# Performance work log

Hardware: AMD Instinct MI355X
Metric: run time of the kernel (lower is better)

Reference implementation:

```python
import jax, jax.numpy as jnp
import numpy as np

NEG_SLOPE = 0.01  # torch F.leaky_relu default


def setup_inputs() -> dict:
    key = jax.random.key(0)
    k1, k2, k3, k4, k5 = jax.random.split(key, 5)
    N, E, IN_DIM, OUT_DIM = 100000, 1600000, 128, 64
    h = jax.random.normal(k1, (N, IN_DIM), dtype=jnp.float32)
    src = jax.random.randint(k2, (E,), 0, N, dtype=jnp.int64)
    dst = jax.random.randint(k3, (E,), 0, N, dtype=jnp.int64)
    # xavier_normal-ish scaled params
    W1 = jax.random.normal(k4, (OUT_DIM, IN_DIM), dtype=jnp.float32) * (2.0 / (IN_DIM + OUT_DIM)) ** 0.5
    Wa = jax.random.normal(k5, (1, 2 * OUT_DIM), dtype=jnp.float32) * (2.0 / (2 * OUT_DIM + 1)) ** 0.5
    return {"h": h, "src": src, "dst": dst, "W1": W1, "Wa": Wa}


def reference(h, src, dst, W1, Wa):
    N = h.shape[0]
    D = W1.shape[0]
    z = h @ W1.T  # [N, D]
    z_src = z[src]  # [E, D] gather
    z_dst = z[dst]  # [E, D] gather
    a_src, a_dst = Wa[0, :D], Wa[0, D:]
    # attn_fc(concat(z_src, z_dst)) == z_src@a_src + z_dst@a_dst
    e = z_src @ a_src + z_dst @ a_dst  # [E]
    e = jnp.where(e >= 0, e, NEG_SLOPE * e)  # leaky_relu
    # segment softmax over incoming edges of each dst node
    e_max = jax.ops.segment_max(e, dst, num_segments=N)
    e_max = jnp.where(jnp.isfinite(e_max), e_max, 0.0)  # empty segments
    e_exp = jnp.exp(e - e_max[dst])
    denom = jax.ops.segment_sum(e_exp, dst, num_segments=N)
    alpha = e_exp / jnp.maximum(denom, 1e-16)[dst]  # [E]
    # weighted scatter-sum of source messages
    h_out = jax.ops.segment_sum(alpha[:, None] * z_src, dst, num_segments=N)  # [N, D]
    return h_out
```

## Files before the change

kernel.cpp:

```cpp
#include <hip/hip_runtime.h>
#include <hip/hip_bf16.h>

#define NEG_SLOPE 0.01f
#define NPB 512
#define CHUNK 2048
#define GROWS 128

typedef __attribute__((ext_vector_type(8))) short short8;
typedef __attribute__((ext_vector_type(4))) float f32x4;

__device__ __forceinline__ unsigned short f2bf_rne(float f) {
    unsigned u = __float_as_uint(f);
    u += 0x7FFFu + ((u >> 16) & 1u);
    return (unsigned short)(u >> 16);
}

__global__ __launch_bounds__(256, 4) void k_gp(
    const float* __restrict__ h, const float* __restrict__ W1,
    const float* __restrict__ Wa, unsigned short* __restrict__ zb,
    float* __restrict__ s, float* __restrict__ t, int N, int G1,
    const int* __restrict__ src, const int* __restrict__ dst,
    unsigned* __restrict__ gcur, unsigned* __restrict__ table,
    int E, int NBKT, int BCAP)
{
    __shared__ __align__(16) union SM {
        struct { short wsb[64 * 128]; short tbuf[4][16 * 64]; } g;
        struct {
            unsigned cnt[256]; unsigned exc[256]; unsigned sbuf[256];
            unsigned gbaseb[256]; unsigned stage[CHUNK];
            unsigned short bkt[CHUNK];
        } p;
    } sm;
    const int tid = threadIdx.x;

    if (blockIdx.x < (unsigned)G1) {
        const int nb = blockIdx.x * GROWS;
        const int w  = tid >> 6;
        const int l  = tid & 63;
        const int lr = l & 15;
        const int lc = l >> 4;
        const int rowbase = nb + w * 32;
        const float4* __restrict__ h4 = (const float4*)h;
        const float4* __restrict__ W14 = (const float4*)W1;

        float asrc[4], adst[4];
#pragma unroll
        for (int ni = 0; ni < 4; ++ni) {
            asrc[ni] = Wa[ni * 16 + lr];
            adst[ni] = Wa[64 + ni * 16 + lr];
        }

        float4 av[8];
        {
            const int myn = rowbase + lr;
#pragma unroll
            for (int ks = 0; ks < 4; ++ks) {
                const int kcb = ks * 4 + lc;
                if (myn < N) {
                    av[2 * ks]     = h4[(size_t)myn * 32 + kcb * 2];
                    av[2 * ks + 1] = h4[(size_t)myn * 32 + kcb * 2 + 1];
                } else {
                    av[2 * ks]     = make_float4(0.f, 0.f, 0.f, 0.f);
                    av[2 * ks + 1] = make_float4(0.f, 0.f, 0.f, 0.f);
                }
            }
        }

#pragma unroll
        for (int it = 0; it < 4; ++it) {
            const int q = tid + it * 256;
            const int r = q >> 4, cb = q & 15;
            float4 v0 = W14[(size_t)r * 32 + cb * 2];
            float4 v1 = W14[(size_t)r * 32 + cb * 2 + 1];
            short8 o;
            o[0]=f2bf_rne(v0.x); o[1]=f2bf_rne(v0.y); o[2]=f2bf_rne(v0.z); o[3]=f2bf_rne(v0.w);
            o[4]=f2bf_rne(v1.x); o[5]=f2bf_rne(v1.y); o[6]=f2bf_rne(v1.z); o[7]=f2bf_rne(v1.w);
            *(short8*)&sm.g.wsb[r * 128 + ((cb * 8) ^ ((r & 7) << 3))] = o;
        }
        __syncthreads();

        short* __restrict__ tb = sm.g.tbuf[w];

#pragma unroll
        for (int rg = 0; rg < 2; ++rg) {
            short8 afr[4];
#pragma unroll
            for (int ks = 0; ks < 4; ++ks) {
                const float4 v0 = av[2 * ks], v1 = av[2 * ks + 1];
                short8 o;
                o[0]=f2bf_rne(v0.x); o[1]=f2bf_rne(v0.y); o[2]=f2bf_rne(v0.z); o[3]=f2bf_rne(v0.w);
                o[4]=f2bf_rne(v1.x); o[5]=f2bf_rne(v1.y); o[6]=f2bf_rne(v1.z); o[7]=f2bf_rne(v1.w);
                afr[ks] = o;
            }
            if (rg < 1) {
                const int myn = rowbase + 16 + lr;
#pragma unroll
                for (int ks = 0; ks < 4; ++ks) {
                    const int kcb = ks * 4 + lc;
                    if (myn < N) {
                        av[2 * ks]     = h4[(size_t)myn * 32 + kcb * 2];
                        av[2 * ks + 1] = h4[(size_t)myn * 32 + kcb * 2 + 1];
                    } else {
                        av[2 * ks]     = make_float4(0.f, 0.f, 0.f, 0.f);
                        av[2 * ks + 1] = make_float4(0.f, 0.f, 0.f, 0.f);
                    }
                }
            }

            f32x4 acc[4];
#pragma unroll
            for (int ni = 0; ni < 4; ++ni) acc[ni] = (f32x4){0.f, 0.f, 0.f, 0.f};
#pragma unroll
            for (int ks = 0; ks < 4; ++ks) {
                const int kcb = ks * 4 + lc;
#pragma unroll
                for (int ni = 0; ni < 4; ++ni) {
                    const int wr = ni * 16 + lr;
                    const short8 bf = *(const short8*)&sm.g.wsb[wr * 128 + ((kcb * 8) ^ ((wr & 7) << 3))];
                    acc[ni] = __builtin_amdgcn_mfma_f32_16x16x32_bf16(afr[ks], bf, acc[ni], 0, 0, 0);
                }
            }

#pragma unroll
            for (int r = 0; r < 4; ++r) {
                float ps = 0.f, pt = 0.f;
#pragma unroll
                for (int ni = 0; ni < 4; ++ni) {
                    ps = fmaf(acc[ni][r], asrc[ni], ps);
                    pt = fmaf(acc[ni][r], adst[ni], pt);
                }
#pragma unroll
                for (int m = 1; m < 16; m <<= 1) {
                    ps += __shfl_xor(ps, m);
                    pt += __shfl_xor(pt, m);
                }
                const int node = rowbase + rg * 16 + lc * 4 + r;
                if (lr == 0 && node < N) { s[node] = ps; t[node] = pt; }
            }

#pragma unroll
            for (int ni = 0; ni < 4; ++ni) {
                const int col = ni * 16 + lr;
#pragma unroll
                for (int r = 0; r < 4; ++r) {
                    const int ro = lc * 4 + r;
                    tb[ro * 64 + (((col >> 3) ^ (ro & 7)) << 3) + (col & 7)]
                        = (short)f2bf_rne(acc[ni][r]);
                }
            }
            {
                const int ro = l >> 2;
                const int n = rowbase + rg * 16 + ro;
                if (n < N) {
#pragma unroll
                    for (int j = 0; j < 2; ++j) {
                        const int c = (l & 3) * 2 + j;
                        const short8 v = *(const short8*)&tb[ro * 64 + ((c ^ (ro & 7)) << 3)];
                        *(short8*)&zb[(size_t)n * 64 + c * 8] = v;
                    }
                }
            }
        }
    } else {
        const int e0 = (blockIdx.x - G1) * CHUNK;
        const int nE = min(CHUNK, E - e0);

        sm.p.cnt[tid] = 0u;
        __syncthreads();
        for (int i = tid; i < nE; i += 256)
            atomicAdd(&sm.p.cnt[(unsigned)dst[e0 + i] >> 9], 1u);
        __syncthreads();

        const unsigned myc = sm.p.cnt[tid];
        if (tid < NBKT && myc > 0u) sm.p.gbaseb[tid] = atomicAdd(&gcur[tid], myc);

        sm.p.sbuf[tid] = myc;
        __syncthreads();
        for (int off = 1; off < 256; off <<= 1) {
            unsigned x = (tid >= off) ? sm.p.sbuf[tid - off] : 0u;
            __syncthreads();
            sm.p.sbuf[tid] += x;
            __syncthreads();
        }
        sm.p.exc[tid] = sm.p.sbuf[tid] - myc;
        __syncthreads();
        sm.p.cnt[tid] = 0u;
        __syncthreads();

        for (int i = tid; i < nE; i += 256) {
            const unsigned d = (unsigned)dst[e0 + i];
            const unsigned b = d >> 9;
            const unsigned pos = sm.p.exc[b] + atomicAdd(&sm.p.cnt[b], 1u);
            sm.p.stage[pos] = ((unsigned)src[e0 + i] << 9) | (d & 511u);
            sm.p.bkt[pos] = (unsigned short)b;
        }
        __syncthreads();

        for (int i = tid; i < nE; i += 256) {
            const unsigned b = sm.p.bkt[i];
            const unsigned off = sm.p.gbaseb[b] + ((unsigned)i - sm.p.exc[b]);
            if (off < (unsigned)BCAP)
                table[(size_t)b * BCAP + off] = sm.p.stage[i];
        }
    }
}

__global__ __launch_bounds__(512) void k_sp(
    const unsigned* __restrict__ table, const unsigned* __restrict__ gcur,
    const float* __restrict__ s, const float* __restrict__ t,
    uint2* __restrict__ edge_ps, unsigned* __restrict__ offsets,
    unsigned* __restrict__ counts, float* __restrict__ invden,
    int N, int NBKT, int BCAP)
{
    __shared__ unsigned ncnt[NPB], nexc[NPB], scur[NPB], sbuf[NPB];
    __shared__ float tlds[NPB], den[NPB];
    __shared__ unsigned basesh;
    const int tid = threadIdx.x;
    const int b = blockIdx.x;
    const int bc = min((int)gcur[b], BCAP);
    const size_t tbo = (size_t)b * BCAP;
    const int node = b * NPB + tid;

    {
        unsigned c = (tid < NBKT) ? min(gcur[tid], (unsigned)BCAP) : 0u;
        sbuf[tid] = c;
        __syncthreads();
        for (int off = 1; off < NPB; off <<= 1) {
            unsigned x = (tid >= off) ? sbuf[tid - off] : 0u;
            __syncthreads();
            sbuf[tid] += x;
            __syncthreads();
        }
        if (tid == 0) basesh = (b == 0) ? 0u : sbuf[b - 1];
    }
    tlds[tid] = (node < N) ? t[node] : 0.f;
    den[tid] = 0.f;
    ncnt[tid] = 0u;
    __syncthreads();
    const unsigned base = basesh;

    for (int i = tid; i < bc; i += NPB)
        atomicAdd(&ncnt[table[tbo + i] & 511u], 1u);
    __syncthreads();

    const unsigned c0 = ncnt[tid];
    sbuf[tid] = c0;
    __syncthreads();
    for (int off = 1; off < NPB; off <<= 1) {
        unsigned x = (tid >= off) ? sbuf[tid - off] : 0u;
        __syncthreads();
        sbuf[tid] += x;
        __syncthreads();
    }
    nexc[tid] = sbuf[tid] - c0;
    scur[tid] = 0u;
    __syncthreads();

    if (node < N) { offsets[node] = base + nexc[tid]; counts[node] = c0; }

    for (int i = tid; i < bc; i += NPB) {
        const unsigned v = table[tbo + i];
        const unsigned l = v & 511u;
        const unsigned sj = v >> 9;
        float e = s[sj] + tlds[l];
        e = (e >= 0.f) ? e : NEG_SLOPE * e;
        const float p = __expf(e);
        const unsigned pos = nexc[l] + atomicAdd(&scur[l], 1u);
        edge_ps[base + pos] = make_uint2(__float_as_uint(p), sj);
        atomicAdd(&den[l], p);
    }
    __syncthreads();
    if (node < N) invden[node] = 1.f / fmaxf(den[tid], 1e-16f);
}

__global__ __launch_bounds__(256) void k_node(
    const unsigned* __restrict__ offsets, const unsigned* __restrict__ counts,
    const uint2* __restrict__ edge_ps, const float* __restrict__ invden,
    const unsigned short* __restrict__ zb, float* __restrict__ out, int N)
{
    const int tid = threadIdx.x;
    const int node = blockIdx.x * 16 + (tid >> 4);
    if (node >= N) return;
    const int wl    = tid & 63;
    const int gbase = wl & ~15;
    const int sub   = wl & 15;
    const int g2    = sub >> 3;
    const int l8    = sub & 7;

    const unsigned beg = offsets[node];
    const int cnt = (int)counts[node];
    if (cnt == 0) {
        if (sub < 8) {
            const float4 zz = make_float4(0.f, 0.f, 0.f, 0.f);
            *(float4*)&out[(size_t)node * 64 + sub * 8]     = zz;
            *(float4*)&out[(size_t)node * 64 + sub * 8 + 4] = zz;
        }
        return;
    }

    const float invd = invden[node];
    const unsigned short* __restrict__ zrow = zb + l8 * 8;
    float acc[8] = {0.f, 0.f, 0.f, 0.f, 0.f, 0.f, 0.f, 0.f};

    for (int base = 0; base < cnt; base += 16) {
        const int rem = cnt - base;
        uint2 ep = make_uint2(0u, 0u);
        if (sub < rem) ep = edge_ps[beg + base + sub];
        const float p = __uint_as_float(ep.x);
        const int  sj = (int)ep.y;

        uint4 vv[8];
#pragma unroll
        for (int k = 0; k < 8; ++k) {
            const int sjj = __shfl(sj, gbase + g2 * 8 + k);
            vv[k] = *(const uint4*)&zrow[(size_t)sjj * 64];
        }
#pragma unroll
        for (int k = 0; k < 8; ++k) {
            const float pj = __shfl(p, gbase + g2 * 8 + k);
            const uint4 v = vv[k];
#define UNPK(u, d0) \
            acc[d0]     = fmaf(pj, __uint_as_float((u) << 16),          acc[d0]); \
            acc[d0 + 1] = fmaf(pj, __uint_as_float((u) & 0xFFFF0000u), acc[d0 + 1]);
            UNPK(v.x, 0) UNPK(v.y, 2) UNPK(v.z, 4) UNPK(v.w, 6)
#undef UNPK
        }
    }

#pragma unroll
    for (int c = 0; c < 8; ++c)
        acc[c] += __shfl_xor(acc[c], 8);

    if (sub < 8) {
        float4 o0 = make_float4(acc[0] * invd, acc[1] * invd, acc[2] * invd, acc[3] * invd);
        float4 o1 = make_float4(acc[4] * invd, acc[5] * invd, acc[6] * invd, acc[7] * invd);
        *(float4*)&out[(size_t)node * 64 + sub * 8]     = o0;
        *(float4*)&out[(size_t)node * 64 + sub * 8 + 4] = o1;
    }
}

extern "C" void kernel_launch(void* const* d_in, const int* in_sizes, int n_in,
                              void* d_out, int out_size, void* d_ws, size_t ws_size,
                              hipStream_t stream) {
    const float* h   = (const float*)d_in[0];
    const int*   src = (const int*)d_in[1];
    const int*   dst = (const int*)d_in[2];
    const float* W1  = (const float*)d_in[3];
    const float* Wa  = (const float*)d_in[4];
    float* out = (float*)d_out;

    const int N = in_sizes[0] / 128;
    const int E = in_sizes[1];
    const int NBKT = (N + NPB - 1) / NPB;
    const int meanb = (E + NBKT - 1) / NBKT;
    int slack = 24 * (int)sqrtf((float)meanb) + 64;
    const int BCAP = meanb + slack;

    const int G1 = (N + GROWS - 1) / GROWS;
    const int G2 = (E + CHUNK - 1) / CHUNK;

    unsigned short* zb = (unsigned short*)d_ws;
    float*    s        = (float*)(zb + (size_t)N * 64);
    float*    t        = s + N;
    unsigned* gcur     = (unsigned*)(t + N);
    unsigned* offsets  = gcur + NBKT;
    unsigned* counts   = offsets + N;
    float*    invden   = (float*)(counts + N);
    uint2*    edge_ps  = (uint2*)(invden + N);
    unsigned* table    = (unsigned*)(edge_ps + E);

    hipMemsetAsync(gcur, 0, (size_t)NBKT * sizeof(unsigned), stream);

    k_gp<<<G1 + G2, 256, 0, stream>>>(h, W1, Wa, zb, s, t, N, G1,
                                      src, dst, gcur, table, E, NBKT, BCAP);
    k_sp<<<NBKT, 512, 0, stream>>>(table, gcur, s, t, edge_ps, offsets, counts,
                                   invden, N, NBKT, BCAP);
    k_node<<<(N + 15) / 16, 256, 0, stream>>>(offsets, counts, edge_ps, invden, zb, out, N);
}
```

Measured before the change: 97.62 us.

## Interleave GEMM and partition blocks and replace LDS scans with wave shuffles

Block indices of the fused kernel now alternate between the GEMM/projection role and the edge-bucketing role, so both kinds of work run concurrently instead of in two sequential phases of the grid. The barrier-heavy Hillis-Steele shared-memory scans in both kernels become wave-level shuffle scans plus a small per-wave total combine, which cuts many __syncthreads. The launch-bounds occupancy hint on k_gp is also lowered from 4 to 2 blocks per SM, which may change register allocation.

```diff
diff --git a/kernel.cpp b/kernel.cpp
--- a/kernel.cpp
+++ b/kernel.cpp
@@ -15,26 +15,41 @@
     return (unsigned short)(u >> 16);
 }
 
-__global__ __launch_bounds__(256, 4) void k_gp(
+__device__ __forceinline__ unsigned wscan_incl(unsigned v) {
+    const int ln = threadIdx.x & 63;
+#pragma unroll
+    for (int off = 1; off < 64; off <<= 1) {
+        unsigned x = __shfl_up(v, off);
+        if (ln >= off) v += x;
+    }
+    return v;
+}
+
+__global__ __launch_bounds__(256, 2) void k_gp(
     const float* __restrict__ h, const float* __restrict__ W1,
     const float* __restrict__ Wa, unsigned short* __restrict__ zb,
     float* __restrict__ s, float* __restrict__ t, int N, int G1,
     const int* __restrict__ src, const int* __restrict__ dst,
     unsigned* __restrict__ gcur, unsigned* __restrict__ table,
-    int E, int NBKT, int BCAP)
+    int E, int NBKT, int BCAP, int minG)
 {
     __shared__ __align__(16) union SM {
         struct { short wsb[64 * 128]; short tbuf[4][16 * 64]; } g;
         struct {
-            unsigned cnt[256]; unsigned exc[256]; unsigned sbuf[256];
-            unsigned gbaseb[256]; unsigned stage[CHUNK];
-            unsigned short bkt[CHUNK];
+            unsigned cnt[256]; unsigned exc[256]; unsigned gbaseb[256];
+            unsigned wtot[4];
+            unsigned stage[CHUNK]; unsigned short bkt[CHUNK];
         } p;
     } sm;
     const int tid = threadIdx.x;
-
-    if (blockIdx.x < (unsigned)G1) {
-        const int nb = blockIdx.x * GROWS;
+    const int bid = blockIdx.x;
+
+    int role, idx;
+    if (bid < 2 * minG) { role = bid & 1; idx = bid >> 1; }
+    else { role = (G1 > minG) ? 0 : 1; idx = minG + (bid - 2 * minG); }
+
+    if (role == 0) {
+        const int nb = idx * GROWS;
         const int w  = tid >> 6;
         const int l  = tid & 63;
         const int lr = l & 15;
@@ -162,7 +177,7 @@
             }
         }
     } else {
-        const int e0 = (blockIdx.x - G1) * CHUNK;
+        const int e0 = idx * CHUNK;
         const int nE = min(CHUNK, E - e0);
 
         sm.p.cnt[tid] = 0u;
@@ -174,17 +189,18 @@
         const unsigned myc = sm.p.cnt[tid];
         if (tid < NBKT && myc > 0u) sm.p.gbaseb[tid] = atomicAdd(&gcur[tid], myc);
 
-        sm.p.sbuf[tid] = myc;
-        __syncthreads();
-        for (int off = 1; off < 256; off <<= 1) {
-            unsigned x = (tid >= off) ? sm.p.sbuf[tid - off] : 0u;
-            __syncthreads();
-            sm.p.sbuf[tid] += x;
-            __syncthreads();
-        }
-        sm.p.exc[tid] = sm.p.sbuf[tid] - myc;
-        __syncthreads();
+        const unsigned inc = wscan_incl(myc);
+        if ((tid & 63) == 63) sm.p.wtot[tid >> 6] = inc;
         sm.p.cnt[tid] = 0u;
+        __syncthreads();
+        {
+            unsigned wo = 0;
+            const int mw = tid >> 6;
+#pragma unroll
+            for (int ww = 0; ww < 4; ++ww)
+                if (ww < mw) wo += sm.p.wtot[ww];
+            sm.p.exc[tid] = wo + inc - myc;
+        }
         __syncthreads();
 
         for (int i = tid; i < nE; i += 256) {
@@ -212,8 +228,9 @@
     unsigned* __restrict__ counts, float* __restrict__ invden,
     int N, int NBKT, int BCAP)
 {
-    __shared__ unsigned ncnt[NPB], nexc[NPB], scur[NPB], sbuf[NPB];
+    __shared__ unsigned ncnt[NPB], nexc[NPB], scur[NPB];
     __shared__ float tlds[NPB], den[NPB];
+    __shared__ unsigned wtot[8];
     __shared__ unsigned basesh;
     const int tid = threadIdx.x;
     const int b = blockIdx.x;
@@ -223,15 +240,15 @@
 
     {
         unsigned c = (tid < NBKT) ? min(gcur[tid], (unsigned)BCAP) : 0u;
-        sbuf[tid] = c;
-        __syncthreads();
-        for (int off = 1; off < NPB; off <<= 1) {
-            unsigned x = (tid >= off) ? sbuf[tid - off] : 0u;
-            __syncthreads();
-            sbuf[tid] += x;
-            __syncthreads();
-        }
-        if (tid == 0) basesh = (b == 0) ? 0u : sbuf[b - 1];
+        const unsigned inc = wscan_incl(c);
+        if ((tid & 63) == 63) wtot[tid >> 6] = inc;
+        __syncthreads();
+        unsigned wo = 0;
+        const int mw = tid >> 6;
+#pragma unroll
+        for (int ww = 0; ww < 8; ++ww)
+            if (ww < mw) wo += wtot[ww];
+        if (tid == b) basesh = wo + inc - c;
     }
     tlds[tid] = (node < N) ? t[node] : 0.f;
     den[tid] = 0.f;
@@ -244,16 +261,18 @@
     __syncthreads();
 
     const unsigned c0 = ncnt[tid];
-    sbuf[tid] = c0;
-    __syncthreads();
-    for (int off = 1; off < NPB; off <<= 1) {
-        unsigned x = (tid >= off) ? sbuf[tid - off] : 0u;
-        __syncthreads();
-        sbuf[tid] += x;
-        __syncthreads();
-    }
-    nexc[tid] = sbuf[tid] - c0;
-    scur[tid] = 0u;
+    {
+        const unsigned inc = wscan_incl(c0);
+        if ((tid & 63) == 63) wtot[tid >> 6] = inc;
+        scur[tid] = 0u;
+        __syncthreads();
+        unsigned wo = 0;
+        const int mw = tid >> 6;
+#pragma unroll
+        for (int ww = 0; ww < 8; ++ww)
+            if (ww < mw) wo += wtot[ww];
+        nexc[tid] = wo + inc - c0;
+    }
     __syncthreads();
 
     if (node < N) { offsets[node] = base + nexc[tid]; counts[node] = c0; }
@@ -358,6 +377,7 @@
 
     const int G1 = (N + GROWS - 1) / GROWS;
     const int G2 = (E + CHUNK - 1) / CHUNK;
+    const int minG = (G1 < G2) ? G1 : G2;
 
     unsigned short* zb = (unsigned short*)d_ws;
     float*    s        = (float*)(zb + (size_t)N * 64);
@@ -372,7 +392,7 @@
     hipMemsetAsync(gcur, 0, (size_t)NBKT * sizeof(unsigned), stream);
 
     k_gp<<<G1 + G2, 256, 0, stream>>>(h, W1, Wa, zb, s, t, N, G1,
-                                      src, dst, gcur, table, E, NBKT, BCAP);
+                                      src, dst, gcur, table, E, NBKT, BCAP, minG);
     k_sp<<<NBKT, 512, 0, stream>>>(table, gcur, s, t, edge_ps, offsets, counts,
                                    invden, N, NBKT, BCAP);
     k_node<<<(N + 15) / 16, 256, 0, stream>>>(offsets, counts, edge_ps, invden, zb, out, N);
```

After: 96.62 us. About the same (-1.0%).

## Load W1 fragments directly into registers and halve GEMM rows per block

Applied to the files above, without the earlier changes.

The projection GEMM branch no longer stages the bf16-converted W1 into shared memory behind a block barrier. Each lane now loads and converts its own W1 MFMA fragments straight from global memory into 16 registers. Each block handles 64 rows, one 16-row tile per wave, instead of 128 rows with a two-step register prefetch loop, and the launch-bounds occupancy hint drops from 4 to 3. The aim is to remove the LDS staging, the __syncthreads and the LDS fragment reads. In exchange it adds more redundant W1 global reads per lane, more register pressure, and doubles the number of GEMM blocks.

```diff
diff --git a/kernel.cpp b/kernel.cpp
--- a/kernel.cpp
+++ b/kernel.cpp
@@ -4,7 +4,7 @@
 #define NEG_SLOPE 0.01f
 #define NPB 512
 #define CHUNK 2048
-#define GROWS 128
+#define GROWS 64
 
 typedef __attribute__((ext_vector_type(8))) short short8;
 typedef __attribute__((ext_vector_type(4))) float f32x4;
@@ -15,7 +15,14 @@
     return (unsigned short)(u >> 16);
 }
 
-__global__ __launch_bounds__(256, 4) void k_gp(
+__device__ __forceinline__ short8 cvt2(float4 v0, float4 v1) {
+    short8 o;
+    o[0]=f2bf_rne(v0.x); o[1]=f2bf_rne(v0.y); o[2]=f2bf_rne(v0.z); o[3]=f2bf_rne(v0.w);
+    o[4]=f2bf_rne(v1.x); o[5]=f2bf_rne(v1.y); o[6]=f2bf_rne(v1.z); o[7]=f2bf_rne(v1.w);
+    return o;
+}
+
+__global__ __launch_bounds__(256, 3) void k_gp(
     const float* __restrict__ h, const float* __restrict__ W1,
     const float* __restrict__ Wa, unsigned short* __restrict__ zb,
     float* __restrict__ s, float* __restrict__ t, int N, int G1,
@@ -24,7 +31,7 @@
     int E, int NBKT, int BCAP)
 {
     __shared__ __align__(16) union SM {
-        struct { short wsb[64 * 128]; short tbuf[4][16 * 64]; } g;
+        short tbuf[4][16 * 64];
         struct {
             unsigned cnt[256]; unsigned exc[256]; unsigned sbuf[256];
             unsigned gbaseb[256]; unsigned stage[CHUNK];
@@ -34,93 +41,57 @@
     const int tid = threadIdx.x;
 
     if (blockIdx.x < (unsigned)G1) {
-        const int nb = blockIdx.x * GROWS;
         const int w  = tid >> 6;
         const int l  = tid & 63;
         const int lr = l & 15;
         const int lc = l >> 4;
-        const int rowbase = nb + w * 32;
+        const int rowbase = blockIdx.x * GROWS + w * 16;
+        const int myn = rowbase + lr;
         const float4* __restrict__ h4 = (const float4*)h;
         const float4* __restrict__ W14 = (const float4*)W1;
 
-        float asrc[4], adst[4];
-#pragma unroll
-        for (int ni = 0; ni < 4; ++ni) {
-            asrc[ni] = Wa[ni * 16 + lr];
-            adst[ni] = Wa[64 + ni * 16 + lr];
-        }
-
         float4 av[8];
+#pragma unroll
+        for (int ks = 0; ks < 4; ++ks) {
+            const int kcb = ks * 4 + lc;
+            if (myn < N) {
+                av[2 * ks]     = h4[(size_t)myn * 32 + kcb * 2];
+                av[2 * ks + 1] = h4[(size_t)myn * 32 + kcb * 2 + 1];
+            } else {
+                av[2 * ks]     = make_float4(0.f, 0.f, 0.f, 0.f);
+                av[2 * ks + 1] = make_float4(0.f, 0.f, 0.f, 0.f);
+            }
+        }
+
+        short8 bf[16];
+#pragma unroll
+        for (int ni = 0; ni < 4; ++ni)
+#pragma unroll
+            for (int ks = 0; ks < 4; ++ks) {
+                const size_t base = (size_t)(ni * 16 + lr) * 32 + (ks * 4 + lc) * 2;
+                bf[ni * 4 + ks] = cvt2(W14[base], W14[base + 1]);
+            }
+
+        short8 afr[4];
+#pragma unroll
+        for (int ks = 0; ks < 4; ++ks) afr[ks] = cvt2(av[2 * ks], av[2 * ks + 1]);
+
+        f32x4 acc[4];
+#pragma unroll
+        for (int ni = 0; ni < 4; ++ni) acc[ni] = (f32x4){0.f, 0.f, 0.f, 0.f};
+#pragma unroll
+        for (int ks = 0; ks < 4; ++ks)
+#pragma unroll
+            for (int ni = 0; ni < 4; ++ni)
+                acc[ni] = __builtin_amdgcn_mfma_f32_16x16x32_bf16(afr[ks], bf[ni * 4 + ks], acc[ni], 0, 0, 0);
+
         {
-            const int myn = rowbase + lr;
-#pragma unroll
-            for (int ks = 0; ks < 4; ++ks) {
-                const int kcb = ks * 4 + lc;
-                if (myn < N) {
-                    av[2 * ks]     = h4[(size_t)myn * 32 + kcb * 2];
-                    av[2 * ks + 1] = h4[(size_t)myn * 32 + kcb * 2 + 1];
-                } else {
-                    av[2 * ks]     = make_float4(0.f, 0.f, 0.f, 0.f);
-                    av[2 * ks + 1] = make_float4(0.f, 0.f, 0.f, 0.f);
-                }
-            }
-        }
-
-#pragma unroll
-        for (int it = 0; it < 4; ++it) {
-            const int q = tid + it * 256;
-            const int r = q >> 4, cb = q & 15;
-            float4 v0 = W14[(size_t)r * 32 + cb * 2];
-            float4 v1 = W14[(size_t)r * 32 + cb * 2 + 1];
-            short8 o;
-            o[0]=f2bf_rne(v0.x); o[1]=f2bf_rne(v0.y); o[2]=f2bf_rne(v0.z); o[3]=f2bf_rne(v0.w);
-            o[4]=f2bf_rne(v1.x); o[5]=f2bf_rne(v1.y); o[6]=f2bf_rne(v1.z); o[7]=f2bf_rne(v1.w);
-            *(short8*)&sm.g.wsb[r * 128 + ((cb * 8) ^ ((r & 7) << 3))] = o;
-        }
-        __syncthreads();
-
-        short* __restrict__ tb = sm.g.tbuf[w];
-
-#pragma unroll
-        for (int rg = 0; rg < 2; ++rg) {
-            short8 afr[4];
-#pragma unroll
-            for (int ks = 0; ks < 4; ++ks) {
-                const float4 v0 = av[2 * ks], v1 = av[2 * ks + 1];
-                short8 o;
-                o[0]=f2bf_rne(v0.x); o[1]=f2bf_rne(v0.y); o[2]=f2bf_rne(v0.z); o[3]=f2bf_rne(v0.w);
-                o[4]=f2bf_rne(v1.x); o[5]=f2bf_rne(v1.y); o[6]=f2bf_rne(v1.z); o[7]=f2bf_rne(v1.w);
-                afr[ks] = o;
-            }
-            if (rg < 1) {
-                const int myn = rowbase + 16 + lr;
-#pragma unroll
-                for (int ks = 0; ks < 4; ++ks) {
-                    const int kcb = ks * 4 + lc;
-                    if (myn < N) {
-                        av[2 * ks]     = h4[(size_t)myn * 32 + kcb * 2];
-                        av[2 * ks + 1] = h4[(size_t)myn * 32 + kcb * 2 + 1];
-                    } else {
-                        av[2 * ks]     = make_float4(0.f, 0.f, 0.f, 0.f);
-                        av[2 * ks + 1] = make_float4(0.f, 0.f, 0.f, 0.f);
-                    }
-                }
-            }
-
-            f32x4 acc[4];
-#pragma unroll
-            for (int ni = 0; ni < 4; ++ni) acc[ni] = (f32x4){0.f, 0.f, 0.f, 0.f};
-#pragma unroll
-            for (int ks = 0; ks < 4; ++ks) {
-                const int kcb = ks * 4 + lc;
-#pragma unroll
-                for (int ni = 0; ni < 4; ++ni) {
-                    const int wr = ni * 16 + lr;
-                    const short8 bf = *(const short8*)&sm.g.wsb[wr * 128 + ((kcb * 8) ^ ((wr & 7) << 3))];
-                    acc[ni] = __builtin_amdgcn_mfma_f32_16x16x32_bf16(afr[ks], bf, acc[ni], 0, 0, 0);
-                }
-            }
-
+            float asrc[4], adst[4];
+#pragma unroll
+            for (int ni = 0; ni < 4; ++ni) {
+                asrc[ni] = Wa[ni * 16 + lr];
+                adst[ni] = Wa[64 + ni * 16 + lr];
+            }
 #pragma unroll
             for (int r = 0; r < 4; ++r) {
                 float ps = 0.f, pt = 0.f;
@@ -134,10 +105,13 @@
                     ps += __shfl_xor(ps, m);
                     pt += __shfl_xor(pt, m);
                 }
-                const int node = rowbase + rg * 16 + lc * 4 + r;
+                const int node = rowbase + lc * 4 + r;
                 if (lr == 0 && node < N) { s[node] = ps; t[node] = pt; }
             }
-
+        }
+
+        {
+            short* __restrict__ tb = sm.tbuf[w];
 #pragma unroll
             for (int ni = 0; ni < 4; ++ni) {
                 const int col = ni * 16 + lr;
@@ -148,16 +122,14 @@
                         = (short)f2bf_rne(acc[ni][r]);
                 }
             }
-            {
-                const int ro = l >> 2;
-                const int n = rowbase + rg * 16 + ro;
-                if (n < N) {
-#pragma unroll
-                    for (int j = 0; j < 2; ++j) {
-                        const int c = (l & 3) * 2 + j;
-                        const short8 v = *(const short8*)&tb[ro * 64 + ((c ^ (ro & 7)) << 3)];
-                        *(short8*)&zb[(size_t)n * 64 + c * 8] = v;
-                    }
+            const int ro = l >> 2;
+            const int n = rowbase + ro;
+            if (n < N) {
+#pragma unroll
+                for (int j = 0; j < 2; ++j) {
+                    const int c = (l & 3) * 2 + j;
+                    const short8 v = *(const short8*)&tb[ro * 64 + ((c ^ (ro & 7)) << 3)];
+                    *(short8*)&zb[(size_t)n * 64 + c * 8] = v;
                 }
             }
         }
```

New measurement: 119.6 us. 1.23x slower.
